# Performance work log

Measured on AMD Instinct MI355X. Metric: run time of the kernel, lower is better.

Reference implementation:

```python
import jax, jax.numpy as jnp
import numpy as np

LN_EPS = 1e-5

def _layernorm(x, gamma, beta):
    mu = jnp.mean(x, axis=-1, keepdims=True)
    var = jnp.mean(jnp.square(x - mu), axis=-1, keepdims=True)
    return (x - mu) * jax.lax.rsqrt(var + LN_EPS) * gamma + beta

def setup_inputs() -> dict:
    key = jax.random.key(0)
    ks = jax.random.split(key, 10)
    d_model, outdim = 1024, 512
    n_support, n_queries = 8192, 8192
    s = 1.0 / np.sqrt(d_model)
    return {
        "support_set": jax.random.normal(ks[0], (n_support, d_model), jnp.float32),
        "queries": jax.random.normal(ks[1], (n_queries, d_model), jnp.float32),
        "Wq": jax.random.uniform(ks[2], (outdim, d_model), jnp.float32, -s, s),
        "bq": jax.random.uniform(ks[3], (outdim,), jnp.float32, -s, s),
        "Wk": jax.random.uniform(ks[4], (outdim, d_model), jnp.float32, -s, s),
        "bk": jax.random.uniform(ks[5], (outdim,), jnp.float32, -s, s),
        "Wv": jax.random.uniform(ks[6], (outdim, d_model), jnp.float32, -s, s),
        "bv": jax.random.uniform(ks[7], (outdim,), jnp.float32, -s, s),
        "ln_gamma": jnp.ones((outdim,), jnp.float32),
        "ln_beta": jnp.zeros((outdim,), jnp.float32),
    }

def reference(support_set, queries, Wq, bq, Wk, bk, Wv, bv, ln_gamma, ln_beta):
    outdim = Wq.shape[0]
    # V projections
    support_vs = support_set @ Wv.T + bv            # [Ns, O]
    q_prototype = queries @ Wv.T + bv               # [Nq, O]
    # QK projections, shared LayerNorm (norm_k applied to both)
    support_ks = _layernorm(support_set @ Wk.T + bk, ln_gamma, ln_beta)  # [Ns, O]
    queries_qs = _layernorm(queries @ Wq.T + bq, ln_gamma, ln_beta)     # [Nq, O]
    # scaled scores + softmax over support axis (dim=1)
    scores = (queries_qs @ support_ks.T) / jnp.sqrt(jnp.float32(outdim))  # [Nq, Ns]
    affinity = jax.nn.softmax(scores, axis=1)
    class_prototype = affinity @ support_vs         # [Nq, O]
    return (q_prototype, class_prototype)
```

## Files before the change

### kernel.cpp

```cpp
#include <hip/hip_runtime.h>
#include <hip/hip_bf16.h>

typedef __attribute__((ext_vector_type(8))) short bf16x8;
typedef __attribute__((ext_vector_type(4))) float f32x4;
typedef __attribute__((ext_vector_type(4))) short short4_t;
typedef __attribute__((ext_vector_type(8))) short short8_t;
typedef __attribute__((ext_vector_type(4))) float float4_t;

#define MFMA16(a, b, c) __builtin_amdgcn_mfma_f32_16x16x32_bf16((a), (b), (c), 0, 0, 0)

__device__ __forceinline__ unsigned short f2bf(float f) {
    unsigned u = __builtin_bit_cast(unsigned, f);
    u += 0x7fffu + ((u >> 16) & 1u);
    return (unsigned short)(u >> 16);
}

__device__ __forceinline__ short4_t pack4(float4_t v) {
    short4_t r;
    r[0] = (short)f2bf(v[0]);
    r[1] = (short)f2bf(v[1]);
    r[2] = (short)f2bf(v[2]);
    r[3] = (short)f2bf(v[3]);
    return r;
}

__device__ __forceinline__ void gload_lds16(const void* g, void* l) {
    __builtin_amdgcn_global_load_lds(
        (const __attribute__((address_space(1))) unsigned int*)g,
        (__attribute__((address_space(3))) unsigned int*)l, 16, 0, 0);
}

__global__ __launch_bounds__(256) void cast_kernel(
    const float* __restrict__ support, const float* __restrict__ queries,
    const float* __restrict__ Wq, const float* __restrict__ Wk,
    const float* __restrict__ Wv,
    unsigned short* __restrict__ sb, unsigned short* __restrict__ qb,
    unsigned short* __restrict__ wqb, unsigned short* __restrict__ wkb,
    unsigned short* __restrict__ wvb)
{
    const size_t e = ((size_t)blockIdx.x * 256 + threadIdx.x) * 8;
    const float* src; unsigned short* dst; size_t off;
    if (e < 8388608)       { src = support; dst = sb;  off = e; }
    else if (e < 16777216) { src = queries; dst = qb;  off = e - 8388608; }
    else if (e < 17301504) { src = Wq;      dst = wqb; off = e - 16777216; }
    else if (e < 17825792) { src = Wk;      dst = wkb; off = e - 17301504; }
    else                   { src = Wv;      dst = wvb; off = e - 17825792; }
    float4_t a = *(const float4_t*)(src + off);
    float4_t b = *(const float4_t*)(src + off + 4);
    short4_t lo = pack4(a), hi = pack4(b);
    short8_t o;
    o[0] = lo[0]; o[1] = lo[1]; o[2] = lo[2]; o[3] = lo[3];
    o[4] = hi[0]; o[5] = hi[1]; o[6] = hi[2]; o[7] = hi[3];
    *(short8_t*)(dst + off) = o;
}

__global__ __launch_bounds__(512, 2) void proj_v_kernel(
    const unsigned short* __restrict__ sb, const unsigned short* __restrict__ qb,
    const unsigned short* __restrict__ wvb, const float* __restrict__ bv,
    float* __restrict__ q_proto, unsigned short* __restrict__ VsT)
{
    const int mode = blockIdx.x >> 7;
    const int rem = blockIdx.x & 127;
    const int rowbase = (rem >> 1) * 128;
    const int colbase = (rem & 1) * 256;
    const unsigned short* A = mode ? sb : qb;

    const int t = threadIdx.x;
    const int w = t >> 6, l = t & 63, lg = l >> 4, ll = l & 15;
    const int wr = w & 1, wc = w >> 1;
    const int sr = l >> 3, su = l & 7;

    __shared__ unsigned short Alds[2][128][64];
    __shared__ unsigned short Blds[2][256][64];

    f32x4 acc[4][4];
    #pragma unroll
    for (int i = 0; i < 4; ++i)
        #pragma unroll
        for (int j = 0; j < 4; ++j) acc[i][j] = (f32x4){0.f, 0.f, 0.f, 0.f};

    #define PV_STAGE(buf, kt)                                                   \
        {                                                                       \
            const int kc = (kt) * 64;                                           \
            _Pragma("unroll")                                                   \
            for (int g = 0; g < 2; ++g) {                                       \
                const int r0 = w * 16 + g * 8, row = r0 + sr;                   \
                gload_lds16(A + (size_t)(rowbase + row) * 1024 + kc             \
                                + ((su ^ (row & 7)) << 3),                      \
                            &Alds[buf][r0][0]);                                 \
            }                                                                   \
            _Pragma("unroll")                                                   \
            for (int g = 0; g < 4; ++g) {                                       \
                const int r0 = w * 32 + g * 8, row = r0 + sr;                   \
                gload_lds16(wvb + (size_t)(colbase + row) * 1024 + kc           \
                                + ((su ^ (row & 7)) << 3),                      \
                            &Blds[buf][r0][0]);                                 \
            }                                                                   \
        }

    PV_STAGE(0, 0)
    __syncthreads();

    for (int kt = 0; kt < 16; ++kt) {
        const int cur = kt & 1;
        if (kt < 15) PV_STAGE(cur ^ 1, kt + 1)
        #pragma unroll
        for (int ks = 0; ks < 2; ++ks) {
            const int u = ((ks * 4 + lg) ^ (ll & 7)) * 8;
            bf16x8 af[4], bfr[4];
            #pragma unroll
            for (int mf = 0; mf < 4; ++mf)
                af[mf] = *(const bf16x8*)&Alds[cur][wr * 64 + mf * 16 + ll][u];
            #pragma unroll
            for (int nf = 0; nf < 4; ++nf)
                bfr[nf] = *(const bf16x8*)&Blds[cur][wc * 64 + nf * 16 + ll][u];
            #pragma unroll
            for (int mf = 0; mf < 4; ++mf)
                #pragma unroll
                for (int nf = 0; nf < 4; ++nf)
                    acc[mf][nf] = MFMA16(af[mf], bfr[nf], acc[mf][nf]);
        }
        __syncthreads();
    }
    #undef PV_STAGE

    float bvv[4];
    #pragma unroll
    for (int nf = 0; nf < 4; ++nf) bvv[nf] = bv[colbase + wc * 64 + nf * 16 + ll];

    if (mode == 0) {
        #pragma unroll
        for (int mf = 0; mf < 4; ++mf)
            #pragma unroll
            for (int r = 0; r < 4; ++r) {
                const size_t row = rowbase + wr * 64 + mf * 16 + lg * 4 + r;
                #pragma unroll
                for (int nf = 0; nf < 4; ++nf)
                    q_proto[row * 512 + colbase + wc * 64 + nf * 16 + ll] = acc[mf][nf][r] + bvv[nf];
            }
    } else {
        #pragma unroll
        for (int mf = 0; mf < 4; ++mf)
            #pragma unroll
            for (int nf = 0; nf < 4; ++nf) {
                float4_t pv = {acc[mf][nf][0] + bvv[nf], acc[mf][nf][1] + bvv[nf],
                               acc[mf][nf][2] + bvv[nf], acc[mf][nf][3] + bvv[nf]};
                const size_t col = colbase + wc * 64 + nf * 16 + ll;
                *(short4_t*)&VsT[col * 8192 + rowbase + wr * 64 + mf * 16 + lg * 4] = pack4(pv);
            }
    }
}

__global__ __launch_bounds__(512, 2) void proj_ln_kernel(
    const unsigned short* __restrict__ sb, const unsigned short* __restrict__ qb,
    const unsigned short* __restrict__ wkb, const float* __restrict__ bk,
    const unsigned short* __restrict__ wqb, const float* __restrict__ bq,
    const float* __restrict__ gamma, const float* __restrict__ beta,
    unsigned short* __restrict__ Ks, unsigned short* __restrict__ Qs)
{
    const int mode = blockIdx.x >> 7;
    const int rowbase = (blockIdx.x & 127) * 64;
    const unsigned short* A = mode ? qb : sb;
    const unsigned short* W = mode ? wqb : wkb;
    const float* bias = mode ? bq : bk;
    unsigned short* dst = mode ? Qs : Ks;

    const int t = threadIdx.x;
    const int w = t >> 6, l = t & 63, lg = l >> 4, ll = l & 15;
    const int sr = l >> 3, su = l & 7;

    __shared__ unsigned short Alds[2][64][64];
    __shared__ unsigned short Blds[2][512][64];
    __shared__ float red[8][64][2];
    __shared__ float stats[64][2];

    f32x4 acc[4][4];
    #pragma unroll
    for (int i = 0; i < 4; ++i)
        #pragma unroll
        for (int j = 0; j < 4; ++j) acc[i][j] = (f32x4){0.f, 0.f, 0.f, 0.f};

    #define LN_STAGE(buf, kt)                                                   \
        {                                                                       \
            const int kc = (kt) * 64;                                           \
            {                                                                   \
                const int r0 = w * 8, row = r0 + sr;                            \
                gload_lds16(A + (size_t)(rowbase + row) * 1024 + kc             \
                                + ((su ^ (row & 7)) << 3),                      \
                            &Alds[buf][r0][0]);                                 \
            }                                                                   \
            _Pragma("unroll")                                                   \
            for (int g = 0; g < 8; ++g) {                                       \
                const int r0 = w * 64 + g * 8, row = r0 + sr;                   \
                gload_lds16(W + (size_t)row * 1024 + kc                         \
                                + ((su ^ (row & 7)) << 3),                      \
                            &Blds[buf][r0][0]);                                 \
            }                                                                   \
        }

    LN_STAGE(0, 0)
    __syncthreads();

    for (int kt = 0; kt < 16; ++kt) {
        const int cur = kt & 1;
        if (kt < 15) LN_STAGE(cur ^ 1, kt + 1)
        #pragma unroll
        for (int ks = 0; ks < 2; ++ks) {
            const int u = ((ks * 4 + lg) ^ (ll & 7)) * 8;
            bf16x8 af[4], bfr[4];
            #pragma unroll
            for (int mf = 0; mf < 4; ++mf)
                af[mf] = *(const bf16x8*)&Alds[cur][mf * 16 + ll][u];
            #pragma unroll
            for (int nf = 0; nf < 4; ++nf)
                bfr[nf] = *(const bf16x8*)&Blds[cur][w * 64 + nf * 16 + ll][u];
            #pragma unroll
            for (int mf = 0; mf < 4; ++mf)
                #pragma unroll
                for (int nf = 0; nf < 4; ++nf)
                    acc[mf][nf] = MFMA16(af[mf], bfr[nf], acc[mf][nf]);
        }
        __syncthreads();
    }
    #undef LN_STAGE

    float bvv[4];
    #pragma unroll
    for (int nf = 0; nf < 4; ++nf) bvv[nf] = bias[w * 64 + nf * 16 + ll];

    float v[4][4][4];
    #pragma unroll
    for (int mf = 0; mf < 4; ++mf)
        #pragma unroll
        for (int nf = 0; nf < 4; ++nf)
            #pragma unroll
            for (int r = 0; r < 4; ++r)
                v[mf][nf][r] = acc[mf][nf][r] + bvv[nf];

    #pragma unroll
    for (int mf = 0; mf < 4; ++mf)
        #pragma unroll
        for (int r = 0; r < 4; ++r) {
            float s = 0.f, q = 0.f;
            #pragma unroll
            for (int nf = 0; nf < 4; ++nf) { s += v[mf][nf][r]; q += v[mf][nf][r] * v[mf][nf][r]; }
            #pragma unroll
            for (int d = 1; d < 16; d <<= 1) { s += __shfl_xor(s, d); q += __shfl_xor(q, d); }
            if (ll == 0) {
                red[w][mf * 16 + lg * 4 + r][0] = s;
                red[w][mf * 16 + lg * 4 + r][1] = q;
            }
        }
    __syncthreads();
    if (t < 64) {
        float S = 0.f, Q = 0.f;
        #pragma unroll
        for (int w2 = 0; w2 < 8; ++w2) { S += red[w2][t][0]; Q += red[w2][t][1]; }
        const float mu = S * (1.f / 512.f);
        const float var = Q * (1.f / 512.f) - mu * mu;
        stats[t][0] = mu;
        stats[t][1] = rsqrtf(var + 1e-5f);
    }
    __syncthreads();
    float gv[4], bev[4];
    #pragma unroll
    for (int nf = 0; nf < 4; ++nf) {
        gv[nf] = gamma[w * 64 + nf * 16 + ll];
        bev[nf] = beta[w * 64 + nf * 16 + ll];
    }
    #pragma unroll
    for (int mf = 0; mf < 4; ++mf)
        #pragma unroll
        for (int r = 0; r < 4; ++r) {
            const int row = mf * 16 + lg * 4 + r;
            const float mu = stats[row][0], rs = stats[row][1];
            #pragma unroll
            for (int nf = 0; nf < 4; ++nf) {
                const float o = (v[mf][nf][r] - mu) * rs * gv[nf] + bev[nf];
                dst[(size_t)(rowbase + row) * 512 + w * 64 + nf * 16 + ll] = f2bf(o);
            }
        }
}

__global__ __launch_bounds__(512, 1) void attn_kernel(
    const unsigned short* __restrict__ Qs, const unsigned short* __restrict__ Ks,
    const unsigned short* __restrict__ VsT,
    float* __restrict__ Opart, float* __restrict__ lpart)
{
    const int bid = blockIdx.x;
    const int sp = (bid & 7) >> 2;
    const int qb = (bid >> 3) * 4 + (bid & 3);
    const int qbase = qb * 64;
    const int kv0 = sp * 4096;
    const int t = threadIdx.x;
    const int w = t >> 6, l = t & 63, lg = l >> 4, ll = l & 15;
    const int wq2 = w & 1, wk4 = w >> 1;

    __shared__ unsigned short Klds[2][64][512];
    __shared__ unsigned short Plds[2][64][64];
    __shared__ float lsum[4][64];

    bf16x8 qf[2][16];
    #pragma unroll
    for (int mf = 0; mf < 2; ++mf) {
        const unsigned short* qrow = Qs + (size_t)(qbase + wq2 * 32 + mf * 16 + ll) * 512 + lg * 8;
        #pragma unroll
        for (int ks = 0; ks < 16; ++ks)
            qf[mf][ks] = *(const bf16x8*)(qrow + ks * 32);
    }

    f32x4 oacc[4][4];
    #pragma unroll
    for (int i = 0; i < 4; ++i)
        #pragma unroll
        for (int j = 0; j < 4; ++j) oacc[i][j] = (f32x4){0.f, 0.f, 0.f, 0.f};
    float lrun[2][4];
    #pragma unroll
    for (int i = 0; i < 2; ++i)
        #pragma unroll
        for (int j = 0; j < 4; ++j) lrun[i][j] = 0.f;
    const float scale = 0.044194173824159216f;

    #pragma unroll
    for (int rr = 0; rr < 8; ++rr) {
        const int r = w * 8 + rr;
        gload_lds16(Ks + (size_t)(kv0 + r) * 512 + ((l ^ (r & 7)) << 3),
                    &Klds[0][r][0]);
    }
    __syncthreads();

    for (int it = 0; it < 64; ++it) {
        const int cur = it & 1;
        const int kvb = kv0 + it * 64;

        if (it < 63) {
            const int kvn = kvb + 64;
            #pragma unroll
            for (int rr = 0; rr < 8; ++rr) {
                const int r = w * 8 + rr;
                gload_lds16(Ks + (size_t)(kvn + r) * 512 + ((l ^ (r & 7)) << 3),
                            &Klds[cur ^ 1][r][0]);
            }
        }

        f32x4 sacc[2];
        sacc[0] = (f32x4){0.f, 0.f, 0.f, 0.f};
        sacc[1] = (f32x4){0.f, 0.f, 0.f, 0.f};
        __builtin_amdgcn_s_setprio(1);
        #pragma unroll
        for (int ks = 0; ks < 16; ++ks) {
            const int u = ((ks * 4 + lg) ^ (ll & 7)) * 8;
            bf16x8 kf = *(const bf16x8*)&Klds[cur][wk4 * 16 + ll][u];
            sacc[0] = MFMA16(qf[0][ks], kf, sacc[0]);
            sacc[1] = MFMA16(qf[1][ks], kf, sacc[1]);
        }
        __builtin_amdgcn_s_setprio(0);

        #pragma unroll
        for (int mf = 0; mf < 2; ++mf)
            #pragma unroll
            for (int r = 0; r < 4; ++r) {
                const int row = wq2 * 32 + mf * 16 + lg * 4 + r;
                const int swz = (row >> 1) & 7;
                const float p = __expf(sacc[mf][r] * scale);
                const int col = wk4 * 16 + ll;
                const int unit = (col >> 3) ^ swz;
                Plds[cur][row][unit * 8 + (col & 7)] = f2bf(p);
                lrun[mf][r] += p;
            }

        __syncthreads();

        __builtin_amdgcn_s_setprio(1);
        #pragma unroll
        for (int ks2 = 0; ks2 < 2; ++ks2) {
            bf16x8 vf[4];
            #pragma unroll
            for (int nf = 0; nf < 4; ++nf)
                vf[nf] = *(const bf16x8*)(VsT + (size_t)(w * 64 + nf * 16 + ll) * 8192
                                          + kvb + ks2 * 32 + lg * 8);
            #pragma unroll
            for (int mf = 0; mf < 4; ++mf) {
                const int row = mf * 16 + ll;
                const int unit = (ks2 * 4 + lg) ^ ((row >> 1) & 7);
                bf16x8 pf = *(const bf16x8*)&Plds[cur][row][unit * 8];
                #pragma unroll
                for (int nf = 0; nf < 4; ++nf)
                    oacc[mf][nf] = MFMA16(pf, vf[nf], oacc[mf][nf]);
            }
        }
        __builtin_amdgcn_s_setprio(0);
    }

    const size_t obase = (size_t)sp * 8192 + qbase;
    #pragma unroll
    for (int mf = 0; mf < 4; ++mf)
        #pragma unroll
        for (int r = 0; r < 4; ++r) {
            const size_t row = obase + mf * 16 + lg * 4 + r;
            #pragma unroll
            for (int nf = 0; nf < 4; ++nf)
                Opart[row * 512 + w * 64 + nf * 16 + ll] = oacc[mf][nf][r];
        }

    #pragma unroll
    for (int mf = 0; mf < 2; ++mf)
        #pragma unroll
        for (int r = 0; r < 4; ++r) {
            float val = lrun[mf][r];
            #pragma unroll
            for (int d = 1; d < 16; d <<= 1) val += __shfl_xor(val, d);
            if (ll == 0)
                lsum[wk4][wq2 * 32 + mf * 16 + lg * 4 + r] = val;
        }
    __syncthreads();
    if (t < 64)
        lpart[(size_t)sp * 8192 + qbase + t] =
            lsum[0][t] + lsum[1][t] + lsum[2][t] + lsum[3][t];
}

__global__ __launch_bounds__(256) void merge_kernel(
    const float* __restrict__ Opart, const float* __restrict__ lpart,
    float* __restrict__ out2)
{
    const int idx = blockIdx.x * 256 + threadIdx.x;
    const int q = idx >> 7;
    const int c = (idx & 127) * 4;
    float4_t a = {0.f, 0.f, 0.f, 0.f};
    float ls = 0.f;
    #pragma unroll
    for (int s = 0; s < 2; ++s) {
        float4_t vv = *(const float4_t*)(Opart + ((size_t)s * 8192 + q) * 512 + c);
        a += vv;
        ls += lpart[s * 8192 + q];
    }
    const float inv = 1.f / ls;
    *(float4_t*)(out2 + (size_t)q * 512 + c) = a * inv;
}

extern "C" void kernel_launch(void* const* d_in, const int* in_sizes, int n_in,
                              void* d_out, int out_size, void* d_ws, size_t ws_size,
                              hipStream_t stream)
{
    const float* support = (const float*)d_in[0];
    const float* queries = (const float*)d_in[1];
    const float* Wq = (const float*)d_in[2];
    const float* bq = (const float*)d_in[3];
    const float* Wk = (const float*)d_in[4];
    const float* bk = (const float*)d_in[5];
    const float* Wv = (const float*)d_in[6];
    const float* bv = (const float*)d_in[7];
    const float* gamma = (const float*)d_in[8];
    const float* beta = (const float*)d_in[9];

    float* out = (float*)d_out;
    float* q_proto = out;
    float* out2 = out + (size_t)8192 * 512;

    char* ws = (char*)d_ws;
    unsigned short* Qs  = (unsigned short*)(ws);
    unsigned short* Ks  = (unsigned short*)(ws + ((size_t)8 << 20));
    unsigned short* VsT = (unsigned short*)(ws + ((size_t)16 << 20));
    unsigned short* sb  = (unsigned short*)(ws + ((size_t)24 << 20));
    unsigned short* qbuf= (unsigned short*)(ws + ((size_t)40 << 20));
    unsigned short* wqb = (unsigned short*)(ws + ((size_t)56 << 20));
    unsigned short* wkb = (unsigned short*)(ws + ((size_t)57 << 20));
    unsigned short* wvb = (unsigned short*)(ws + ((size_t)58 << 20));
    float* Opart = (float*)(ws + ((size_t)24 << 20));
    float* lpart = (float*)(ws + ((size_t)59 << 20));

    cast_kernel<<<8960, 256, 0, stream>>>(support, queries, Wq, Wk, Wv,
                                          sb, qbuf, wqb, wkb, wvb);
    proj_v_kernel<<<256, 512, 0, stream>>>(sb, qbuf, wvb, bv, q_proto, VsT);
    proj_ln_kernel<<<256, 512, 0, stream>>>(sb, qbuf, wkb, bk, wqb, bq,
                                            gamma, beta, Ks, Qs);
    attn_kernel<<<256, 512, 0, stream>>>(Qs, Ks, VsT, Opart, lpart);
    merge_kernel<<<4096, 256, 0, stream>>>(Opart, lpart, out2);
}
```

Baseline: 361.7 us.

## Software-pipeline QK^T of next tile with PV of current tile in attention

Restructures the attention loop so the QK^T MFMAs for the next KV tile are interleaved with the P·V MFMAs for the current tile, with a prologue computing the first scores and an epilogue doing the last PV. Wave mapping changes from 2x4 to 4x2 (each wave handles 16 query rows and 32 keys), V fragments are loaded before the K prefetch, and launch bounds ask for 2 blocks per CU. The goal is to hide exp/LDS latency behind matrix work and cut one barrier's stall per iteration. The cost is higher register pressure, which the occupancy hint may make worse, and more complex code.

```diff
diff --git a/kernel.cpp b/kernel.cpp
--- a/kernel.cpp
+++ b/kernel.cpp
@@ -282,7 +282,7 @@
         }
 }
 
-__global__ __launch_bounds__(512, 1) void attn_kernel(
+__global__ __launch_bounds__(512, 2) void attn_kernel(
     const unsigned short* __restrict__ Qs, const unsigned short* __restrict__ Ks,
     const unsigned short* __restrict__ VsT,
     float* __restrict__ Opart, float* __restrict__ lpart)
@@ -294,19 +294,18 @@
     const int kv0 = sp * 4096;
     const int t = threadIdx.x;
     const int w = t >> 6, l = t & 63, lg = l >> 4, ll = l & 15;
-    const int wq2 = w & 1, wk4 = w >> 1;
+    const int wq = w & 3, wk = w >> 2;
 
     __shared__ unsigned short Klds[2][64][512];
     __shared__ unsigned short Plds[2][64][64];
-    __shared__ float lsum[4][64];
-
-    bf16x8 qf[2][16];
-    #pragma unroll
-    for (int mf = 0; mf < 2; ++mf) {
-        const unsigned short* qrow = Qs + (size_t)(qbase + wq2 * 32 + mf * 16 + ll) * 512 + lg * 8;
+    __shared__ float lsum[2][64];
+
+    bf16x8 qf[16];
+    {
+        const unsigned short* qrow = Qs + (size_t)(qbase + wq * 16 + ll) * 512 + lg * 8;
         #pragma unroll
         for (int ks = 0; ks < 16; ++ks)
-            qf[mf][ks] = *(const bf16x8*)(qrow + ks * 32);
+            qf[ks] = *(const bf16x8*)(qrow + ks * 32);
     }
 
     f32x4 oacc[4][4];
@@ -314,64 +313,101 @@
     for (int i = 0; i < 4; ++i)
         #pragma unroll
         for (int j = 0; j < 4; ++j) oacc[i][j] = (f32x4){0.f, 0.f, 0.f, 0.f};
-    float lrun[2][4];
-    #pragma unroll
-    for (int i = 0; i < 2; ++i)
-        #pragma unroll
-        for (int j = 0; j < 4; ++j) lrun[i][j] = 0.f;
+    float lrun[4] = {0.f, 0.f, 0.f, 0.f};
     const float scale = 0.044194173824159216f;
 
-    #pragma unroll
-    for (int rr = 0; rr < 8; ++rr) {
-        const int r = w * 8 + rr;
-        gload_lds16(Ks + (size_t)(kv0 + r) * 512 + ((l ^ (r & 7)) << 3),
-                    &Klds[0][r][0]);
-    }
-    __syncthreads();
-
-    for (int it = 0; it < 64; ++it) {
-        const int cur = it & 1;
+    #define K_STAGE(buf, kvt)                                                   \
+        {                                                                       \
+            _Pragma("unroll")                                                   \
+            for (int rr = 0; rr < 8; ++rr) {                                    \
+                const int r = w * 8 + rr;                                       \
+                gload_lds16(Ks + (size_t)((kvt) + r) * 512 + ((l ^ (r & 7)) << 3), \
+                            &Klds[buf][r][0]);                                  \
+            }                                                                   \
+        }
+
+    K_STAGE(0, kv0)
+    __syncthreads();
+    K_STAGE(1, kv0 + 64)
+
+    {
+        f32x4 s0 = (f32x4){0.f, 0.f, 0.f, 0.f}, s1 = (f32x4){0.f, 0.f, 0.f, 0.f};
+        #pragma unroll
+        for (int j = 0; j < 16; ++j) {
+            const int u = ((j * 4 + lg) ^ (ll & 7)) * 8;
+            bf16x8 ka = *(const bf16x8*)&Klds[0][wk * 32 + ll][u];
+            bf16x8 kb = *(const bf16x8*)&Klds[0][wk * 32 + 16 + ll][u];
+            s0 = MFMA16(qf[j], ka, s0);
+            s1 = MFMA16(qf[j], kb, s1);
+        }
+        #pragma unroll
+        for (int r = 0; r < 4; ++r) {
+            const int row = wq * 16 + lg * 4 + r;
+            const int swz = (row >> 1) & 7;
+            const float p0 = __expf(s0[r] * scale);
+            const float p1 = __expf(s1[r] * scale);
+            const int c0 = wk * 32 + ll, c1 = c0 + 16;
+            Plds[0][row][(((c0 >> 3) ^ swz) << 3) + (c0 & 7)] = f2bf(p0);
+            Plds[0][row][(((c1 >> 3) ^ swz) << 3) + (c1 & 7)] = f2bf(p1);
+            lrun[r] += p0 + p1;
+        }
+    }
+    __syncthreads();
+
+    for (int it = 0; it < 63; ++it) {
+        const int cur = it & 1, nxt = cur ^ 1;
         const int kvb = kv0 + it * 64;
 
-        if (it < 63) {
-            const int kvn = kvb + 64;
-            #pragma unroll
-            for (int rr = 0; rr < 8; ++rr) {
-                const int r = w * 8 + rr;
-                gload_lds16(Ks + (size_t)(kvn + r) * 512 + ((l ^ (r & 7)) << 3),
-                            &Klds[cur ^ 1][r][0]);
+        bf16x8 vf[2][4];
+        #pragma unroll
+        for (int ks2 = 0; ks2 < 2; ++ks2)
+            #pragma unroll
+            for (int nf = 0; nf < 4; ++nf)
+                vf[ks2][nf] = *(const bf16x8*)(VsT + (size_t)(w * 64 + nf * 16 + ll) * 8192
+                                               + kvb + ks2 * 32 + lg * 8);
+        if (it < 62) K_STAGE(cur, kvb + 128)
+
+        f32x4 s0 = (f32x4){0.f, 0.f, 0.f, 0.f}, s1 = (f32x4){0.f, 0.f, 0.f, 0.f};
+        bf16x8 pf;
+        __builtin_amdgcn_s_setprio(1);
+        #pragma unroll
+        for (int j = 0; j < 16; ++j) {
+            const int u = ((j * 4 + lg) ^ (ll & 7)) * 8;
+            bf16x8 ka = *(const bf16x8*)&Klds[nxt][wk * 32 + ll][u];
+            bf16x8 kb = *(const bf16x8*)&Klds[nxt][wk * 32 + 16 + ll][u];
+            s0 = MFMA16(qf[j], ka, s0);
+            s1 = MFMA16(qf[j], kb, s1);
+            #pragma unroll
+            for (int s = 0; s < 2; ++s) {
+                const int f = 2 * j + s;
+                const int ks2 = f >> 4, mf = (f >> 2) & 3, nf = f & 3;
+                if (nf == 0) {
+                    const int row = mf * 16 + ll;
+                    const int unit = (ks2 * 4 + lg) ^ ((row >> 1) & 7);
+                    pf = *(const bf16x8*)&Plds[cur][row][unit * 8];
+                }
+                oacc[mf][nf] = MFMA16(pf, vf[ks2][nf], oacc[mf][nf]);
             }
         }
-
-        f32x4 sacc[2];
-        sacc[0] = (f32x4){0.f, 0.f, 0.f, 0.f};
-        sacc[1] = (f32x4){0.f, 0.f, 0.f, 0.f};
-        __builtin_amdgcn_s_setprio(1);
-        #pragma unroll
-        for (int ks = 0; ks < 16; ++ks) {
-            const int u = ((ks * 4 + lg) ^ (ll & 7)) * 8;
-            bf16x8 kf = *(const bf16x8*)&Klds[cur][wk4 * 16 + ll][u];
-            sacc[0] = MFMA16(qf[0][ks], kf, sacc[0]);
-            sacc[1] = MFMA16(qf[1][ks], kf, sacc[1]);
-        }
         __builtin_amdgcn_s_setprio(0);
 
         #pragma unroll
-        for (int mf = 0; mf < 2; ++mf)
-            #pragma unroll
-            for (int r = 0; r < 4; ++r) {
-                const int row = wq2 * 32 + mf * 16 + lg * 4 + r;
-                const int swz = (row >> 1) & 7;
-                const float p = __expf(sacc[mf][r] * scale);
-                const int col = wk4 * 16 + ll;
-                const int unit = (col >> 3) ^ swz;
-                Plds[cur][row][unit * 8 + (col & 7)] = f2bf(p);
-                lrun[mf][r] += p;
-            }
-
+        for (int r = 0; r < 4; ++r) {
+            const int row = wq * 16 + lg * 4 + r;
+            const int swz = (row >> 1) & 7;
+            const float p0 = __expf(s0[r] * scale);
+            const float p1 = __expf(s1[r] * scale);
+            const int c0 = wk * 32 + ll, c1 = c0 + 16;
+            Plds[nxt][row][(((c0 >> 3) ^ swz) << 3) + (c0 & 7)] = f2bf(p0);
+            Plds[nxt][row][(((c1 >> 3) ^ swz) << 3) + (c1 & 7)] = f2bf(p1);
+            lrun[r] += p0 + p1;
+        }
         __syncthreads();
-
-        __builtin_amdgcn_s_setprio(1);
+    }
+    #undef K_STAGE
+
+    {
+        const int kvb = kv0 + 63 * 64;
         #pragma unroll
         for (int ks2 = 0; ks2 < 2; ++ks2) {
             bf16x8 vf[4];
@@ -383,13 +419,12 @@
             for (int mf = 0; mf < 4; ++mf) {
                 const int row = mf * 16 + ll;
                 const int unit = (ks2 * 4 + lg) ^ ((row >> 1) & 7);
-                bf16x8 pf = *(const bf16x8*)&Plds[cur][row][unit * 8];
+                bf16x8 pf = *(const bf16x8*)&Plds[1][row][unit * 8];
                 #pragma unroll
                 for (int nf = 0; nf < 4; ++nf)
                     oacc[mf][nf] = MFMA16(pf, vf[nf], oacc[mf][nf]);
             }
         }
-        __builtin_amdgcn_s_setprio(0);
     }
 
     const size_t obase = (size_t)sp * 8192 + qbase;
@@ -404,19 +439,16 @@
         }
 
     #pragma unroll
-    for (int mf = 0; mf < 2; ++mf)
-        #pragma unroll
-        for (int r = 0; r < 4; ++r) {
-            float val = lrun[mf][r];
-            #pragma unroll
-            for (int d = 1; d < 16; d <<= 1) val += __shfl_xor(val, d);
-            if (ll == 0)
-                lsum[wk4][wq2 * 32 + mf * 16 + lg * 4 + r] = val;
-        }
+    for (int r = 0; r < 4; ++r) {
+        float val = lrun[r];
+        #pragma unroll
+        for (int d = 1; d < 16; d <<= 1) val += __shfl_xor(val, d);
+        if (ll == 0)
+            lsum[wk][wq * 16 + lg * 4 + r] = val;
+    }
     __syncthreads();
     if (t < 64)
-        lpart[(size_t)sp * 8192 + qbase + t] =
-            lsum[0][t] + lsum[1][t] + lsum[2][t] + lsum[3][t];
+        lpart[(size_t)sp * 8192 + qbase + t] = lsum[0][t] + lsum[1][t];
 }
 
 __global__ __launch_bounds__(256) void merge_kernel(
```

Measured after the change: 337.6 us. 1.07x faster.

## Split attention into 32-query blocks of 256 threads with single-buffered K

Applied to the files above, without the earlier changes.

The attention kernel now uses 512 blocks of 4 waves, each handling 32 queries instead of 64, and K tiles are single-buffered in shared memory. The prefetch of the next K tile is issued after the score barrier, and explicit waitcnt and s_barrier calls order the loads. Each wave now covers 128 output columns with 8 V fragments per step. The goal is to fit more blocks per CU and raise occupancy, at the cost of loading K twice as often across all blocks and less overlap from losing the double buffer.

```diff
diff --git a/kernel.cpp b/kernel.cpp
--- a/kernel.cpp
+++ b/kernel.cpp
@@ -282,7 +282,7 @@
         }
 }
 
-__global__ __launch_bounds__(512, 1) void attn_kernel(
+__global__ __launch_bounds__(256) void attn_kernel(
     const unsigned short* __restrict__ Qs, const unsigned short* __restrict__ Ks,
     const unsigned short* __restrict__ VsT,
     float* __restrict__ Opart, float* __restrict__ lpart)
@@ -290,30 +290,29 @@
     const int bid = blockIdx.x;
     const int sp = (bid & 7) >> 2;
     const int qb = (bid >> 3) * 4 + (bid & 3);
-    const int qbase = qb * 64;
+    const int qbase = qb * 32;
     const int kv0 = sp * 4096;
     const int t = threadIdx.x;
     const int w = t >> 6, l = t & 63, lg = l >> 4, ll = l & 15;
-    const int wq2 = w & 1, wk4 = w >> 1;
-
-    __shared__ unsigned short Klds[2][64][512];
-    __shared__ unsigned short Plds[2][64][64];
-    __shared__ float lsum[4][64];
+
+    __shared__ unsigned short Klds[64][512];
+    __shared__ unsigned short Plds[32][64];
+    __shared__ float lsum[4][32];
 
     bf16x8 qf[2][16];
     #pragma unroll
     for (int mf = 0; mf < 2; ++mf) {
-        const unsigned short* qrow = Qs + (size_t)(qbase + wq2 * 32 + mf * 16 + ll) * 512 + lg * 8;
+        const unsigned short* qrow = Qs + (size_t)(qbase + mf * 16 + ll) * 512 + lg * 8;
         #pragma unroll
         for (int ks = 0; ks < 16; ++ks)
             qf[mf][ks] = *(const bf16x8*)(qrow + ks * 32);
     }
 
-    f32x4 oacc[4][4];
-    #pragma unroll
-    for (int i = 0; i < 4; ++i)
-        #pragma unroll
-        for (int j = 0; j < 4; ++j) oacc[i][j] = (f32x4){0.f, 0.f, 0.f, 0.f};
+    f32x4 oacc[2][8];
+    #pragma unroll
+    for (int i = 0; i < 2; ++i)
+        #pragma unroll
+        for (int j = 0; j < 8; ++j) oacc[i][j] = (f32x4){0.f, 0.f, 0.f, 0.f};
     float lrun[2][4];
     #pragma unroll
     for (int i = 0; i < 2; ++i)
@@ -321,86 +320,103 @@
         for (int j = 0; j < 4; ++j) lrun[i][j] = 0.f;
     const float scale = 0.044194173824159216f;
 
-    #pragma unroll
-    for (int rr = 0; rr < 8; ++rr) {
-        const int r = w * 8 + rr;
-        gload_lds16(Ks + (size_t)(kv0 + r) * 512 + ((l ^ (r & 7)) << 3),
-                    &Klds[0][r][0]);
-    }
+    #define K_STAGE(kvt)                                                        \
+        {                                                                       \
+            _Pragma("unroll")                                                   \
+            for (int rr = 0; rr < 16; ++rr) {                                   \
+                const int r = w * 16 + rr;                                      \
+                gload_lds16(Ks + (size_t)((kvt) + r) * 512 + ((l ^ (r & 7)) << 3), \
+                            &Klds[r][0]);                                       \
+            }                                                                   \
+        }
+
+    K_STAGE(kv0)
     __syncthreads();
 
     for (int it = 0; it < 64; ++it) {
-        const int cur = it & 1;
         const int kvb = kv0 + it * 64;
 
-        if (it < 63) {
-            const int kvn = kvb + 64;
-            #pragma unroll
-            for (int rr = 0; rr < 8; ++rr) {
-                const int r = w * 8 + rr;
-                gload_lds16(Ks + (size_t)(kvn + r) * 512 + ((l ^ (r & 7)) << 3),
-                            &Klds[cur ^ 1][r][0]);
-            }
-        }
-
-        f32x4 sacc[2];
-        sacc[0] = (f32x4){0.f, 0.f, 0.f, 0.f};
-        sacc[1] = (f32x4){0.f, 0.f, 0.f, 0.f};
+        f32x4 sacc0 = (f32x4){0.f, 0.f, 0.f, 0.f};
+        f32x4 sacc1 = (f32x4){0.f, 0.f, 0.f, 0.f};
         __builtin_amdgcn_s_setprio(1);
         #pragma unroll
         for (int ks = 0; ks < 16; ++ks) {
             const int u = ((ks * 4 + lg) ^ (ll & 7)) * 8;
-            bf16x8 kf = *(const bf16x8*)&Klds[cur][wk4 * 16 + ll][u];
-            sacc[0] = MFMA16(qf[0][ks], kf, sacc[0]);
-            sacc[1] = MFMA16(qf[1][ks], kf, sacc[1]);
+            bf16x8 kf = *(const bf16x8*)&Klds[w * 16 + ll][u];
+            sacc0 = MFMA16(qf[0][ks], kf, sacc0);
+            sacc1 = MFMA16(qf[1][ks], kf, sacc1);
         }
         __builtin_amdgcn_s_setprio(0);
 
-        #pragma unroll
-        for (int mf = 0; mf < 2; ++mf)
+        __syncthreads();
+
+        if (it < 63) K_STAGE(kvb + 64)
+
+        bf16x8 vf0[8];
+        #pragma unroll
+        for (int nf = 0; nf < 8; ++nf)
+            vf0[nf] = *(const bf16x8*)(VsT + (size_t)(w * 128 + nf * 16 + ll) * 8192
+                                       + kvb + lg * 8);
+
+        #pragma unroll
+        for (int mf = 0; mf < 2; ++mf) {
+            const f32x4 sa = mf ? sacc1 : sacc0;
             #pragma unroll
             for (int r = 0; r < 4; ++r) {
-                const int row = wq2 * 32 + mf * 16 + lg * 4 + r;
-                const int swz = (row >> 1) & 7;
-                const float p = __expf(sacc[mf][r] * scale);
-                const int col = wk4 * 16 + ll;
-                const int unit = (col >> 3) ^ swz;
-                Plds[cur][row][unit * 8 + (col & 7)] = f2bf(p);
+                const int row = mf * 16 + lg * 4 + r;
+                const float p = __expf(sa[r] * scale);
+                const int col = w * 16 + ll;
+                const int unit = (col >> 3) ^ ((row >> 1) & 3);
+                Plds[row][unit * 8 + (col & 7)] = f2bf(p);
                 lrun[mf][r] += p;
             }
-
-        __syncthreads();
+        }
+
+        asm volatile("s_waitcnt lgkmcnt(0)" ::: "memory");
+        __builtin_amdgcn_sched_barrier(0);
+        __builtin_amdgcn_s_barrier();
 
         __builtin_amdgcn_s_setprio(1);
         #pragma unroll
-        for (int ks2 = 0; ks2 < 2; ++ks2) {
-            bf16x8 vf[4];
-            #pragma unroll
-            for (int nf = 0; nf < 4; ++nf)
-                vf[nf] = *(const bf16x8*)(VsT + (size_t)(w * 64 + nf * 16 + ll) * 8192
-                                          + kvb + ks2 * 32 + lg * 8);
-            #pragma unroll
-            for (int mf = 0; mf < 4; ++mf) {
-                const int row = mf * 16 + ll;
-                const int unit = (ks2 * 4 + lg) ^ ((row >> 1) & 7);
-                bf16x8 pf = *(const bf16x8*)&Plds[cur][row][unit * 8];
-                #pragma unroll
-                for (int nf = 0; nf < 4; ++nf)
-                    oacc[mf][nf] = MFMA16(pf, vf[nf], oacc[mf][nf]);
-            }
+        for (int mf = 0; mf < 2; ++mf) {
+            const int row = mf * 16 + ll;
+            const int unit = lg ^ ((row >> 1) & 3);
+            bf16x8 pf = *(const bf16x8*)&Plds[row][unit * 8];
+            #pragma unroll
+            for (int nf = 0; nf < 8; ++nf)
+                oacc[mf][nf] = MFMA16(pf, vf0[nf], oacc[mf][nf]);
+        }
+        bf16x8 vf1[8];
+        #pragma unroll
+        for (int nf = 0; nf < 8; ++nf)
+            vf1[nf] = *(const bf16x8*)(VsT + (size_t)(w * 128 + nf * 16 + ll) * 8192
+                                       + kvb + 32 + lg * 8);
+        #pragma unroll
+        for (int mf = 0; mf < 2; ++mf) {
+            const int row = mf * 16 + ll;
+            const int unit = (4 + lg) ^ ((row >> 1) & 3);
+            bf16x8 pf = *(const bf16x8*)&Plds[row][unit * 8];
+            #pragma unroll
+            for (int nf = 0; nf < 8; ++nf)
+                oacc[mf][nf] = MFMA16(pf, vf1[nf], oacc[mf][nf]);
         }
         __builtin_amdgcn_s_setprio(0);
-    }
+
+        asm volatile("s_waitcnt vmcnt(0)" ::: "memory");
+        __builtin_amdgcn_sched_barrier(0);
+        __builtin_amdgcn_s_barrier();
+    }
+    #undef K_STAGE
 
     const size_t obase = (size_t)sp * 8192 + qbase;
     #pragma unroll
-    for (int mf = 0; mf < 4; ++mf)
+    for (int mf = 0; mf < 2; ++mf)
         #pragma unroll
         for (int r = 0; r < 4; ++r) {
             const size_t row = obase + mf * 16 + lg * 4 + r;
             #pragma unroll
-            for (int nf = 0; nf < 4; ++nf)
-                Opart[row * 512 + w * 64 + nf * 16 + ll] = oacc[mf][nf][r];
+            for (int nf = 0; nf < 8; ++nf)
+                Opart[row * 512 + w * 128 + nf * 16 + ll] = oacc[mf][nf][r];
         }
 
     #pragma unroll
@@ -411,10 +427,10 @@
             #pragma unroll
             for (int d = 1; d < 16; d <<= 1) val += __shfl_xor(val, d);
             if (ll == 0)
-                lsum[wk4][wq2 * 32 + mf * 16 + lg * 4 + r] = val;
-        }
-    __syncthreads();
-    if (t < 64)
+                lsum[w][mf * 16 + lg * 4 + r] = val;
+        }
+    __syncthreads();
+    if (t < 32)
         lpart[(size_t)sp * 8192 + qbase + t] =
             lsum[0][t] + lsum[1][t] + lsum[2][t] + lsum[3][t];
 }
@@ -474,6 +490,6 @@
     proj_v_kernel<<<256, 512, 0, stream>>>(sb, qbuf, wvb, bv, q_proto, VsT);
     proj_ln_kernel<<<256, 512, 0, stream>>>(sb, qbuf, wkb, bk, wqb, bq,
                                             gamma, beta, Ks, Qs);
-    attn_kernel<<<256, 512, 0, stream>>>(Qs, Ks, VsT, Opart, lpart);
+    attn_kernel<<<512, 256, 0, stream>>>(Qs, Ks, VsT, Opart, lpart);
     merge_kernel<<<4096, 256, 0, stream>>>(Opart, lpart, out2);
 }
```

Measured after the change: 524.1 us. 44.9% more time.
